# Kernel tuning notes

Hardware: AMD Instinct MI355X
Metric: run time of the kernel (lower is better)

## Reference

```python
import jax, jax.numpy as jnp
import numpy as np
import math

B, S, HID = 1, 2048, 1024
H = 16
D = HID // H          # head_dim = 64
M = 128               # RFF num_features
SIGMA = 1.0
ALPHA = 0.9
NORMALIZE = True


def setup_inputs() -> dict:
    key = jax.random.key(0)
    ks = jax.random.split(key, 12)
    s = 1.0 / math.sqrt(HID)  # nn.Linear default-ish init scale
    inp = {
        "hidden_states": jax.random.normal(ks[0], (B, S, HID), dtype=jnp.float32),
        "attention_mask": jnp.zeros((B, 1, 1, S), dtype=jnp.float32),  # 0 = attend
        "Wq": jax.random.uniform(ks[1], (HID, HID), minval=-s, maxval=s, dtype=jnp.float32),
        "bq": jnp.zeros((HID,), dtype=jnp.float32),
        "Wk": jax.random.uniform(ks[2], (HID, HID), minval=-s, maxval=s, dtype=jnp.float32),
        "bk": jnp.zeros((HID,), dtype=jnp.float32),
        "Wv": jax.random.uniform(ks[3], (HID, HID), minval=-s, maxval=s, dtype=jnp.float32),
        "bv": jnp.zeros((HID,), dtype=jnp.float32),
        "Wo": jax.random.uniform(ks[4], (HID, HID), minval=-s, maxval=s, dtype=jnp.float32),
        "bo": jnp.zeros((HID,), dtype=jnp.float32),
        # RFF kernel params per head: omega ~ N(0, 1/sigma^2), phase b ~ U[0, 2pi]
        "omega": jax.random.normal(ks[5], (H, D, M), dtype=jnp.float32) / SIGMA,
        "rff_b": jax.random.uniform(ks[6], (H, M), minval=0.0, maxval=2.0 * math.pi, dtype=jnp.float32),
    }
    return inp


def _heads(x):
    # (B, S, HID) -> (B, H, S, D)
    return x.reshape(B, S, H, D).transpose(0, 2, 1, 3)


def _phi(x, omega, rff_b):
    # x: (B, H, S, D) -> (B, H, S, M) random Fourier features
    proj = jnp.einsum("bhsd,hdm->bhsm", x, omega) + rff_b[None, :, None, :]
    phi = math.sqrt(2.0 / M) * jnp.cos(proj)
    if NORMALIZE:
        phi = phi / (jnp.linalg.norm(phi, axis=-1, keepdims=True) + 1e-6)
    return phi


def reference(hidden_states, attention_mask, Wq, bq, Wk, bk, Wv, bv, Wo, bo, omega, rff_b):
    q = _heads(hidden_states @ Wq.T + bq)   # (B,H,S,D)
    k = _heads(hidden_states @ Wk.T + bk)
    v = _heads(hidden_states @ Wv.T + bv)

    qn = q / (jnp.linalg.norm(q, axis=-1, keepdims=True) + 1e-6)
    kn = k / (jnp.linalg.norm(k, axis=-1, keepdims=True) + 1e-6)

    dot_scores = jnp.einsum("bhqd,bhkd->bhqk", q, k)             # standard QK^T
    kernel_scores = jnp.einsum("bhqm,bhkm->bhqk",
                               _phi(qn, omega, rff_b),
                               _phi(kn, omega, rff_b))            # phi(Q)phi(K)^T

    scores = (ALPHA * dot_scores + (1.0 - ALPHA) * kernel_scores) / math.sqrt(D)
    scores = scores + attention_mask * -10000.0
    weights = jax.nn.softmax(scores, axis=-1)                     # dropout: eval mode (identity)

    context = jnp.einsum("bhqk,bhkd->bhqd", weights, v)
    context = context.transpose(0, 2, 1, 3).reshape(B, S, HID)
    return context @ Wo.T + bo
```

## Files before the change

kernel.cpp:

```cpp
#include <hip/hip_runtime.h>
#include <math.h>

#define S_LEN 2048
#define HID   1024
#define NH    16
#define HD    64
#define NM    128
#define CAUG  192
#define NCH   32

constexpr float ALPHA = 0.9f;

typedef __attribute__((ext_vector_type(8))) short bf16x8;
typedef __attribute__((ext_vector_type(4))) short bf16x4;
typedef __attribute__((ext_vector_type(4))) float f32x4;
typedef __attribute__((ext_vector_type(4))) int   int4v;

#define MFMA(a,b,c) __builtin_amdgcn_mfma_f32_16x16x32_bf16(a,b,c,0,0,0)

static __device__ inline short f2bf(float f) {
    unsigned u = __float_as_uint(f);
    u += 0x7fffu + ((u >> 16) & 1u);
    return (short)(u >> 16);
}
static __device__ inline float bf2f(short s) {
    return __uint_as_float(((unsigned)(unsigned short)s) << 16);
}

__global__ __launch_bounds__(256)
void conv_kernel(const float* __restrict__ hs,
                 const float* __restrict__ Wq, const float* __restrict__ Wk,
                 const float* __restrict__ Wv, const float* __restrict__ Wo,
                 const float* __restrict__ omega,
                 short* __restrict__ hsb, short* __restrict__ wqb, short* __restrict__ wkb,
                 short* __restrict__ wvb, short* __restrict__ wob, short* __restrict__ omtb)
{
    int i = blockIdx.x * 256 + threadIdx.x;
    if (i >= 1605632) return;
    if (i >= 1572864) {
        int j = (i - 1572864) * 4;
        int h = j >> 13, rem = j & 8191;
        int d = rem >> 7, m = rem & 127;
        float4 v = *(const float4*)(omega + j);
        short* dst = omtb + ((h * 128 + m) << 6) + d;
        dst[0]       = f2bf(v.x);
        dst[64]      = f2bf(v.y);
        dst[128]     = f2bf(v.z);
        dst[192]     = f2bf(v.w);
        return;
    }
    const float* src; short* dst; int off;
    if (i < 524288) { src = hs; dst = hsb; off = i; }
    else {
        int j = i - 524288;
        int r = j >> 18;
        off = j & 262143;
        src = (r == 0) ? Wq : (r == 1) ? Wk : (r == 2) ? Wv : Wo;
        dst = (r == 0) ? wqb : (r == 1) ? wkb : (r == 2) ? wvb : wob;
    }
    float4 v = ((const float4*)src)[off];
    bf16x4 o; o[0] = f2bf(v.x); o[1] = f2bf(v.y); o[2] = f2bf(v.z); o[3] = f2bf(v.w);
    ((bf16x4*)dst)[off] = o;
}

__global__ __launch_bounds__(256)
void gemm_mfma(const short* __restrict__ A,
               const short* __restrict__ W0, const float* __restrict__ b0, void* C0,
               const short* __restrict__ W1, const float* __restrict__ b1, void* C1,
               const short* __restrict__ W2, const float* __restrict__ b2, void* C2,
               int m0_, int m1_, int m2_, int Mrows)
{
    const short* W; const float* bias; void* C; int mode;
    if (blockIdx.z == 0)      { W = W0; bias = b0; C = C0; mode = m0_; }
    else if (blockIdx.z == 1) { W = W1; bias = b1; C = C1; mode = m1_; }
    else                      { W = W2; bias = b2; C = C2; mode = m2_; }

    __shared__ short As[64][40];
    __shared__ short Bs[128][40];

    const int tid = threadIdx.x;
    const int wave = tid >> 6, lane = tid & 63;
    const int l15 = lane & 15, l4 = lane >> 4;
    const int wm = wave >> 1, wn = wave & 1;
    const int m0 = blockIdx.y * 64, n0 = blockIdx.x * 128;

    const int srow = tid >> 2;
    const int scol = (tid & 3) * 16;

    f32x4 acc[2][4];
#pragma unroll
    for (int i = 0; i < 2; ++i)
#pragma unroll
        for (int j = 0; j < 4; ++j) acc[i][j] = (f32x4){0.f,0.f,0.f,0.f};

    int4v apre, bpre0, bpre1;
    apre  = *(const int4v*)((const char*)A + (size_t)(m0 + srow) * 2048 + scol);
    bpre0 = *(const int4v*)((const char*)W + (size_t)(n0 + srow) * 2048 + scol);
    bpre1 = *(const int4v*)((const char*)W + (size_t)(n0 + 64 + srow) * 2048 + scol);

    for (int ks = 0; ks < 32; ++ks) {
        __syncthreads();
        *(int4v*)((char*)&As[0][0] + srow * 80 + scol) = apre;
        *(int4v*)((char*)&Bs[0][0] + srow * 80 + scol) = bpre0;
        *(int4v*)((char*)&Bs[0][0] + (64 + srow) * 80 + scol) = bpre1;
        __syncthreads();
        if (ks + 1 < 32) {
            const int kb = (ks + 1) * 64;
            apre  = *(const int4v*)((const char*)A + (size_t)(m0 + srow) * 2048 + kb + scol);
            bpre0 = *(const int4v*)((const char*)W + (size_t)(n0 + srow) * 2048 + kb + scol);
            bpre1 = *(const int4v*)((const char*)W + (size_t)(n0 + 64 + srow) * 2048 + kb + scol);
        }
        bf16x8 af[2], bf[4];
#pragma unroll
        for (int mi = 0; mi < 2; ++mi)
            af[mi] = *(const bf16x8*)((const char*)&As[0][0] + (wm*32 + mi*16 + l15) * 80 + l4*16);
#pragma unroll
        for (int nj = 0; nj < 4; ++nj)
            bf[nj] = *(const bf16x8*)((const char*)&Bs[0][0] + (wn*64 + nj*16 + l15) * 80 + l4*16);
#pragma unroll
        for (int mi = 0; mi < 2; ++mi)
#pragma unroll
            for (int nj = 0; nj < 4; ++nj)
                acc[mi][nj] = MFMA(af[mi], bf[nj], acc[mi][nj]);
    }

#pragma unroll
    for (int nj = 0; nj < 4; ++nj) {
        const int nglob = n0 + wn*64 + nj*16 + l15;
        const float bn = bias[nglob];
#pragma unroll
        for (int mi = 0; mi < 2; ++mi) {
            const int mbase = m0 + wm*32 + mi*16 + l4*4;
            if (mode == 0) {
#pragma unroll
                for (int r = 0; r < 4; ++r)
                    ((short*)C)[(size_t)(mbase + r) * 1024 + nglob] = f2bf(acc[mi][nj][r] + bn);
            } else if (mode == 1) {
                bf16x4 pk;
#pragma unroll
                for (int r = 0; r < 4; ++r) pk[r] = f2bf(acc[mi][nj][r] + bn);
                *(bf16x4*)((short*)C + (size_t)nglob * Mrows + mbase) = pk;
            } else {
#pragma unroll
                for (int r = 0; r < 4; ++r)
                    ((float*)C)[(size_t)(mbase + r) * 1024 + nglob] = acc[mi][nj][r] + bn;
            }
        }
    }
}

__global__ __launch_bounds__(256)
void phi2_kernel(const short* __restrict__ qbuf, const short* __restrict__ kbuf,
                 const short* __restrict__ omtb, const float* __restrict__ rffb,
                 short* __restrict__ Qa, short* __restrict__ Ka)
{
    __shared__ short om[128][72];
    __shared__ float bsh[128];

    const int src = blockIdx.z, h = blockIdx.y;
    const int s0 = blockIdx.x * 64;
    const short* X = src ? kbuf : qbuf;
    short* Out     = src ? Ka : Qa;
    const float fq   = src ? 1.0f : (ALPHA * 0.125f);
    const float fphi = src ? 1.0f : ((1.0f - ALPHA) * 0.125f);

    const int tid = threadIdx.x, wave = tid >> 6, lane = tid & 63;
    const int l15 = lane & 15, l4 = lane >> 4;

    {
        const char* gsrc = (const char*)(omtb + ((size_t)h << 13));
#pragma unroll
        for (int it = 0; it < 4; ++it) {
            int f = tid * 16 + it * 4096;
            int row = f >> 7, colb = f & 127;
            *(int4v*)((char*)&om[0][0] + row * 144 + colb) = *(const int4v*)(gsrc + f);
        }
        if (tid < 128) bsh[tid] = rffb[h * 128 + tid];
    }
    __syncthreads();

    const int srow = s0 + wave * 16 + l15;

    bf16x8 xf[2];
#pragma unroll
    for (int cs = 0; cs < 2; ++cs)
        xf[cs] = *(const bf16x8*)(X + (size_t)srow * HID + h * HD + cs * 32 + l4 * 8);

    float ss = 0.f;
#pragma unroll
    for (int cs = 0; cs < 2; ++cs)
#pragma unroll
        for (int j = 0; j < 8; ++j) { float v = bf2f(xf[cs][j]); ss = fmaf(v, v, ss); }
    ss += __shfl_xor(ss, 16);
    ss += __shfl_xor(ss, 32);
    const float inv = 1.0f / (sqrtf(ss) + 1e-6f);

    bf16x8 qn[2];
#pragma unroll
    for (int cs = 0; cs < 2; ++cs) {
        bf16x8 o, w;
#pragma unroll
        for (int j = 0; j < 8; ++j) {
            float v = bf2f(xf[cs][j]);
            o[j] = f2bf(v * inv);
            w[j] = f2bf(v * fq);
        }
        qn[cs] = o;
        *(bf16x8*)(Out + ((size_t)h * S_LEN + srow) * CAUG + cs * 32 + l4 * 8) = w;
    }

    f32x4 pacc[8];
#pragma unroll
    for (int t = 0; t < 8; ++t) pacc[t] = (f32x4){0.f,0.f,0.f,0.f};
#pragma unroll
    for (int t = 0; t < 8; ++t)
#pragma unroll
        for (int cs = 0; cs < 2; ++cs) {
            bf16x8 bf = *(const bf16x8*)((const char*)&om[0][0] + (t*16 + l15) * 144 + cs*64 + l4*16);
            pacc[t] = MFMA(qn[cs], bf, pacc[t]);
        }

    float ph[8][4];
    float ps[4] = {0.f, 0.f, 0.f, 0.f};
#pragma unroll
    for (int t = 0; t < 8; ++t) {
        const float bv = bsh[t * 16 + l15];
#pragma unroll
        for (int r = 0; r < 4; ++r) {
            float p = pacc[t][r] + bv;
            float c = 0.125f * __cosf(p);
            ph[t][r] = c;
            ps[r] = fmaf(c, c, ps[r]);
        }
    }
#pragma unroll
    for (int r = 0; r < 4; ++r) {
        ps[r] += __shfl_xor(ps[r], 1);
        ps[r] += __shfl_xor(ps[r], 2);
        ps[r] += __shfl_xor(ps[r], 4);
        ps[r] += __shfl_xor(ps[r], 8);
    }
    float inv2[4];
#pragma unroll
    for (int r = 0; r < 4; ++r) inv2[r] = fphi / (sqrtf(ps[r]) + 1e-6f);

#pragma unroll
    for (int t = 0; t < 8; ++t)
#pragma unroll
        for (int r = 0; r < 4; ++r)
            Out[((size_t)h * S_LEN + s0 + wave * 16 + l4 * 4 + r) * CAUG + 64 + t * 16 + l15]
                = f2bf(ph[t][r] * inv2[r]);
}

__global__ __launch_bounds__(256, 2)
void flash_mfma(const short* __restrict__ Qa, const short* __restrict__ Ka,
                const short* __restrict__ vt, const float* __restrict__ mask,
                short* __restrict__ ctxb)
{
    __shared__ char smem[56320];

    const int tid = threadIdx.x;
    const int wave = tid >> 6, lane = tid & 63;
    const int l15 = lane & 15, l4 = lane >> 4;
    const int g = wave >> 1, sub = wave & 1;
    const int h = blockIdx.y;
    const int q0 = blockIdx.x * 64 + sub * 32;

    char* PlW  = smem + wave * 2560;
    char* Kbuf = smem + 10240 + g * 12800;
    char* Vt0  = smem + 35840 + g * 10240;
    char* Vt1  = Vt0 + 5120;

    bf16x8 qf[2][6];
#pragma unroll
    for (int qj = 0; qj < 2; ++qj)
#pragma unroll
        for (int cs = 0; cs < 6; ++cs)
            qf[qj][cs] = *(const bf16x8*)(Qa + ((size_t)h * 2048 + q0 + qj*16 + l15) * CAUG + cs*32 + l4*8);

    f32x4 oacc[4][2];
#pragma unroll
    for (int di = 0; di < 4; ++di)
#pragma unroll
        for (int qj = 0; qj < 2; ++qj) oacc[di][qj] = (f32x4){0.f,0.f,0.f,0.f};
    float lsum[2] = {0.f, 0.f};

    const int t = tid & 127;
    int kr[6], kcb[6], vr[2], vcb[2];
#pragma unroll
    for (int it = 0; it < 6; ++it) { int f = t*16 + it*2048; kr[it] = f/384; kcb[it] = f%384; }
#pragma unroll
    for (int it = 0; it < 2; ++it) { int f = t*16 + it*2048; vr[it] = f/64; vcb[it] = f%64; }

    const char* Kg = (const char*)(Ka + (size_t)h * 2048 * CAUG);
    const char* Vg = (const char*)(vt + (size_t)h * 64 * 2048);
    const int base = g * NCH;

    int4v kpre[6], vpre[2];
    auto loadPre = [&](int kt) {
        const char* kb = Kg + (size_t)kt * 12288;
#pragma unroll
        for (int it = 0; it < 6; ++it)
            kpre[it] = *(const int4v*)(kb + (size_t)kr[it]*384 + kcb[it]);
#pragma unroll
        for (int it = 0; it < 2; ++it)
            vpre[it] = *(const int4v*)(Vg + (size_t)vr[it]*4096 + kt*64 + vcb[it]);
    };

    f32x4 sacc_p[2][2];
    float4 mkp0, mkp1;

    auto softmax_pv = [&](char* Vbuf) {
#pragma unroll
        for (int fi = 0; fi < 2; ++fi) {
            const float4 mk = fi ? mkp1 : mkp0;
            float mv[4] = {mk.x * -10000.f, mk.y * -10000.f, mk.z * -10000.f, mk.w * -10000.f};
#pragma unroll
            for (int qj = 0; qj < 2; ++qj) {
                bf16x4 pk;
#pragma unroll
                for (int r = 0; r < 4; ++r) {
                    float p = __expf(sacc_p[fi][qj][r] + mv[r]);
                    lsum[qj] += p;
                    pk[r] = f2bf(p);
                }
                *(bf16x4*)(PlW + (qj*16 + l15)*80 + fi*32 + l4*8) = pk;
            }
        }
        bf16x8 va[4], pb[2];
#pragma unroll
        for (int di = 0; di < 4; ++di)
            va[di] = *(const bf16x8*)(Vbuf + (di*16 + l15)*80 + l4*16);
#pragma unroll
        for (int qj = 0; qj < 2; ++qj)
            pb[qj] = *(const bf16x8*)(PlW + (qj*16 + l15)*80 + l4*16);
#pragma unroll
        for (int di = 0; di < 4; ++di)
#pragma unroll
            for (int qj = 0; qj < 2; ++qj)
                oacc[di][qj] = MFMA(va[di], pb[qj], oacc[di][qj]);
    };

    loadPre(base);

    for (int i = 0; i < NCH; ++i) {
        const int kt = base + i;
        char* Vcur = (i & 1) ? Vt1 : Vt0;
        __syncthreads();
#pragma unroll
        for (int it = 0; it < 6; ++it)
            *(int4v*)(Kbuf + kr[it]*400 + kcb[it]) = kpre[it];
#pragma unroll
        for (int it = 0; it < 2; ++it)
            *(int4v*)(Vcur + vr[it]*80 + vcb[it]) = vpre[it];
        __syncthreads();

        f32x4 sc[2][2];
#pragma unroll
        for (int fi = 0; fi < 2; ++fi)
#pragma unroll
            for (int qj = 0; qj < 2; ++qj) sc[fi][qj] = (f32x4){0.f,0.f,0.f,0.f};
#pragma unroll
        for (int cs = 0; cs < 6; ++cs) {
            bf16x8 ka[2];
#pragma unroll
            for (int fi = 0; fi < 2; ++fi)
                ka[fi] = *(const bf16x8*)(Kbuf + (fi*16 + l15)*400 + cs*64 + l4*16);
#pragma unroll
            for (int fi = 0; fi < 2; ++fi)
#pragma unroll
                for (int qj = 0; qj < 2; ++qj)
                    sc[fi][qj] = MFMA(ka[fi], qf[qj][cs], sc[fi][qj]);
        }
        float4 mkc0 = *(const float4*)&mask[kt*32 + l4*4];
        float4 mkc1 = *(const float4*)&mask[kt*32 + 16 + l4*4];

        if (i + 1 < NCH) loadPre(kt + 1);

        if (i > 0) softmax_pv((i & 1) ? Vt0 : Vt1);

#pragma unroll
        for (int fi = 0; fi < 2; ++fi)
#pragma unroll
            for (int qj = 0; qj < 2; ++qj) sacc_p[fi][qj] = sc[fi][qj];
        mkp0 = mkc0; mkp1 = mkc1;
    }
    softmax_pv(Vt1);

#pragma unroll
    for (int qj = 0; qj < 2; ++qj) {
        lsum[qj] += __shfl_xor(lsum[qj], 16);
        lsum[qj] += __shfl_xor(lsum[qj], 32);
    }

    __syncthreads();
    float* scrO = (float*)(smem + 10240);
    float* scrL = (float*)(smem + 27648);
    if (g == 1) {
#pragma unroll
        for (int qj = 0; qj < 2; ++qj) {
#pragma unroll
            for (int di = 0; di < 4; ++di)
                *(f32x4*)&scrO[(size_t)(sub*32 + qj*16 + l15)*68 + di*16 + l4*4] = oacc[di][qj];
            if (l4 == 0) scrL[sub*32 + qj*16 + l15] = lsum[qj];
        }
    }
    __syncthreads();
    if (g == 0) {
#pragma unroll
        for (int qj = 0; qj < 2; ++qj) {
            const float l = lsum[qj] + scrL[sub*32 + qj*16 + l15];
            const float inv = 1.0f / l;
            const int s = q0 + qj*16 + l15;
#pragma unroll
            for (int di = 0; di < 4; ++di) {
                f32x4 o2 = *(const f32x4*)&scrO[(size_t)(sub*32 + qj*16 + l15)*68 + di*16 + l4*4];
                bf16x4 ob;
#pragma unroll
                for (int r = 0; r < 4; ++r) ob[r] = f2bf((oacc[di][qj][r] + o2[r]) * inv);
                *(bf16x4*)(ctxb + (size_t)s * HID + h*64 + di*16 + l4*4) = ob;
            }
        }
    }
}

extern "C" void kernel_launch(void* const* d_in, const int* in_sizes, int n_in,
                              void* d_out, int out_size, void* d_ws, size_t ws_size,
                              hipStream_t stream)
{
    const float* hs    = (const float*)d_in[0];
    const float* mask  = (const float*)d_in[1];
    const float* Wq    = (const float*)d_in[2];
    const float* bq    = (const float*)d_in[3];
    const float* Wk    = (const float*)d_in[4];
    const float* bk    = (const float*)d_in[5];
    const float* Wv    = (const float*)d_in[6];
    const float* bv    = (const float*)d_in[7];
    const float* Wo    = (const float*)d_in[8];
    const float* bo    = (const float*)d_in[9];
    const float* omega = (const float*)d_in[10];
    const float* rffb  = (const float*)d_in[11];
    float* out = (float*)d_out;

    short* wsS = (short*)d_ws;
    short* hsb = wsS;
    short* wqb = hsb + 2097152;
    short* wkb = wqb + 1048576;
    short* wvb = wkb + 1048576;
    short* wob = wvb + 1048576;
    short* qb  = wob + 1048576;
    short* kb  = qb  + 2097152;
    short* vtb = kb  + 2097152;
    short* ctxb= vtb + 2097152;
    short* QaB = ctxb+ 2097152;
    short* KaB = QaB + 6291456;
    short* omtb= KaB + 6291456;

    conv_kernel<<<6272, 256, 0, stream>>>(hs, Wq, Wk, Wv, Wo, omega,
                                          hsb, wqb, wkb, wvb, wob, omtb);
    gemm_mfma<<<dim3(8, 32, 3), 256, 0, stream>>>(hsb, wqb, bq, qb, wkb, bk, kb, wvb, bv, vtb,
                                                  0, 0, 1, S_LEN);
    phi2_kernel<<<dim3(32, 16, 2), 256, 0, stream>>>(qb, kb, omtb, rffb, QaB, KaB);
    flash_mfma<<<dim3(32, 16), 256, 0, stream>>>(QaB, KaB, vtb, mask, ctxb);
    gemm_mfma<<<dim3(8, 32, 1), 256, 0, stream>>>(ctxb, wob, bo, out, wob, bo, out, wob, bo, out,
                                                  2, 2, 2, S_LEN);
}
```

Before: 119.1 us.

## Split flash attention keys across four waves with per-wave private K tiles

Restructures the attention kernel so each of the four waves handles all 64 queries of the block over its own quarter of the key range, in place of two wave groups that each covered half the queries and half the keys. Each wave now stages its K tile in its own XOR-swizzled LDS region, which removes the per-chunk __syncthreads. V fragments are loaded straight from global memory into registers, and the next K tile is written into LDS half by half while the current one is consumed. This cuts block-wide barriers and LDS bank conflicts, at the cost of more registers (64 query rows per wave) and a four-way reduction of partial outputs at the end.

```diff
diff --git a/kernel.cpp b/kernel.cpp
--- a/kernel.cpp
+++ b/kernel.cpp
@@ -7,7 +7,6 @@
 #define HD    64
 #define NM    128
 #define CAUG  192
-#define NCH   32
 
 constexpr float ALPHA = 0.9f;
 
@@ -257,168 +256,158 @@
                 const short* __restrict__ vt, const float* __restrict__ mask,
                 short* __restrict__ ctxb)
 {
-    __shared__ char smem[56320];
+    __shared__ char smem[65536];
 
     const int tid = threadIdx.x;
     const int wave = tid >> 6, lane = tid & 63;
     const int l15 = lane & 15, l4 = lane >> 4;
-    const int g = wave >> 1, sub = wave & 1;
     const int h = blockIdx.y;
-    const int q0 = blockIdx.x * 64 + sub * 32;
-
-    char* PlW  = smem + wave * 2560;
-    char* Kbuf = smem + 10240 + g * 12800;
-    char* Vt0  = smem + 35840 + g * 10240;
-    char* Vt1  = Vt0 + 5120;
-
-    bf16x8 qf[2][6];
-#pragma unroll
-    for (int qj = 0; qj < 2; ++qj)
+    const int q0 = blockIdx.x * 64;
+
+    char* Kbuf = smem + wave * 12288;
+    char* Pb   = smem + 49152 + wave * 4096;
+
+    bf16x8 qf[4][6];
+#pragma unroll
+    for (int qj = 0; qj < 4; ++qj)
 #pragma unroll
         for (int cs = 0; cs < 6; ++cs)
             qf[qj][cs] = *(const bf16x8*)(Qa + ((size_t)h * 2048 + q0 + qj*16 + l15) * CAUG + cs*32 + l4*8);
 
-    f32x4 oacc[4][2];
+    f32x4 oacc[4][4];
 #pragma unroll
     for (int di = 0; di < 4; ++di)
 #pragma unroll
-        for (int qj = 0; qj < 2; ++qj) oacc[di][qj] = (f32x4){0.f,0.f,0.f,0.f};
-    float lsum[2] = {0.f, 0.f};
-
-    const int t = tid & 127;
-    int kr[6], kcb[6], vr[2], vcb[2];
-#pragma unroll
-    for (int it = 0; it < 6; ++it) { int f = t*16 + it*2048; kr[it] = f/384; kcb[it] = f%384; }
-#pragma unroll
-    for (int it = 0; it < 2; ++it) { int f = t*16 + it*2048; vr[it] = f/64; vcb[it] = f%64; }
+        for (int qj = 0; qj < 4; ++qj) oacc[di][qj] = (f32x4){0.f,0.f,0.f,0.f};
+    float lsum[4] = {0.f, 0.f, 0.f, 0.f};
 
     const char* Kg = (const char*)(Ka + (size_t)h * 2048 * CAUG);
     const char* Vg = (const char*)(vt + (size_t)h * 64 * 2048);
-    const int base = g * NCH;
-
-    int4v kpre[6], vpre[2];
-    auto loadPre = [&](int kt) {
-        const char* kb = Kg + (size_t)kt * 12288;
+    const int c0 = wave * 16;
+
+    int wrA[6];
+#pragma unroll
+    for (int it = 0; it < 6; ++it) {
+        int p = it * 1024 + lane * 16;
+        int row = p / 384;
+        int col = p - row * 384;
+        wrA[it] = row * 384 + (col ^ ((row & 7) << 4));
+    }
+
+    int4v kpre[6];
+    bf16x8 va[4];
+
+    auto loadKhalf = [&](int kt, int half) {
+        const char* kb = Kg + (size_t)kt * 12288 + half * 6144;
 #pragma unroll
         for (int it = 0; it < 6; ++it)
-            kpre[it] = *(const int4v*)(kb + (size_t)kr[it]*384 + kcb[it]);
-#pragma unroll
-        for (int it = 0; it < 2; ++it)
-            vpre[it] = *(const int4v*)(Vg + (size_t)vr[it]*4096 + kt*64 + vcb[it]);
+            kpre[it] = *(const int4v*)(kb + it * 1024 + lane * 16);
     };
-
-    f32x4 sacc_p[2][2];
-    float4 mkp0, mkp1;
-
-    auto softmax_pv = [&](char* Vbuf) {
+    auto writeKhalf = [&](int half) {
+        char* b = Kbuf + half * 6144;
+#pragma unroll
+        for (int it = 0; it < 6; ++it)
+            *(int4v*)(b + wrA[it]) = kpre[it];
+    };
+    auto loadV = [&](int kt) {
+#pragma unroll
+        for (int di = 0; di < 4; ++di)
+            va[di] = *(const bf16x8*)(Vg + (size_t)(di*16 + l15)*4096 + kt*64 + l4*16);
+    };
+
+    loadKhalf(c0, 0); writeKhalf(0);
+    loadKhalf(c0, 1); writeKhalf(1);
+    loadV(c0);
+
+    for (int i = 0; i < 16; ++i) {
+        const int kt = c0 + i;
+        const bool more = (i + 1 < 16);
+        if (more) loadKhalf(kt + 1, 0);
+
 #pragma unroll
         for (int fi = 0; fi < 2; ++fi) {
-            const float4 mk = fi ? mkp1 : mkp0;
+            f32x4 sacc[4];
+#pragma unroll
+            for (int qj = 0; qj < 4; ++qj) sacc[qj] = (f32x4){0.f,0.f,0.f,0.f};
+            const int r = fi * 16 + l15;
+            const int sw = (l15 & 7) << 4;
+#pragma unroll
+            for (int cs = 0; cs < 6; ++cs) {
+                bf16x8 ka = *(const bf16x8*)(Kbuf + r * 384 + ((cs*64 + l4*16) ^ sw));
+#pragma unroll
+                for (int qj = 0; qj < 4; ++qj)
+                    sacc[qj] = MFMA(ka, qf[qj][cs], sacc[qj]);
+            }
+            float4 mk = *(const float4*)&mask[kt*32 + fi*16 + l4*4];
             float mv[4] = {mk.x * -10000.f, mk.y * -10000.f, mk.z * -10000.f, mk.w * -10000.f};
 #pragma unroll
-            for (int qj = 0; qj < 2; ++qj) {
+            for (int qj = 0; qj < 4; ++qj) {
                 bf16x4 pk;
 #pragma unroll
-                for (int r = 0; r < 4; ++r) {
-                    float p = __expf(sacc_p[fi][qj][r] + mv[r]);
+                for (int rr = 0; rr < 4; ++rr) {
+                    float p = __expf(sacc[qj][rr] + mv[rr]);
                     lsum[qj] += p;
-                    pk[r] = f2bf(p);
+                    pk[rr] = f2bf(p);
                 }
-                *(bf16x4*)(PlW + (qj*16 + l15)*80 + fi*32 + l4*8) = pk;
+                const int prow = qj*16 + l15;
+                *(bf16x4*)(Pb + prow*64 + ((fi*32 + l4*8) ^ ((prow & 3) << 4))) = pk;
             }
-        }
-        bf16x8 va[4], pb[2];
-#pragma unroll
-        for (int di = 0; di < 4; ++di)
-            va[di] = *(const bf16x8*)(Vbuf + (di*16 + l15)*80 + l4*16);
-#pragma unroll
-        for (int qj = 0; qj < 2; ++qj)
-            pb[qj] = *(const bf16x8*)(PlW + (qj*16 + l15)*80 + l4*16);
-#pragma unroll
-        for (int di = 0; di < 4; ++di)
-#pragma unroll
-            for (int qj = 0; qj < 2; ++qj)
-                oacc[di][qj] = MFMA(va[di], pb[qj], oacc[di][qj]);
-    };
-
-    loadPre(base);
-
-    for (int i = 0; i < NCH; ++i) {
-        const int kt = base + i;
-        char* Vcur = (i & 1) ? Vt1 : Vt0;
-        __syncthreads();
-#pragma unroll
-        for (int it = 0; it < 6; ++it)
-            *(int4v*)(Kbuf + kr[it]*400 + kcb[it]) = kpre[it];
-#pragma unroll
-        for (int it = 0; it < 2; ++it)
-            *(int4v*)(Vcur + vr[it]*80 + vcb[it]) = vpre[it];
-        __syncthreads();
-
-        f32x4 sc[2][2];
-#pragma unroll
-        for (int fi = 0; fi < 2; ++fi)
-#pragma unroll
-            for (int qj = 0; qj < 2; ++qj) sc[fi][qj] = (f32x4){0.f,0.f,0.f,0.f};
-#pragma unroll
-        for (int cs = 0; cs < 6; ++cs) {
-            bf16x8 ka[2];
-#pragma unroll
-            for (int fi = 0; fi < 2; ++fi)
-                ka[fi] = *(const bf16x8*)(Kbuf + (fi*16 + l15)*400 + cs*64 + l4*16);
-#pragma unroll
-            for (int fi = 0; fi < 2; ++fi)
-#pragma unroll
-                for (int qj = 0; qj < 2; ++qj)
-                    sc[fi][qj] = MFMA(ka[fi], qf[qj][cs], sc[fi][qj]);
-        }
-        float4 mkc0 = *(const float4*)&mask[kt*32 + l4*4];
-        float4 mkc1 = *(const float4*)&mask[kt*32 + 16 + l4*4];
-
-        if (i + 1 < NCH) loadPre(kt + 1);
-
-        if (i > 0) softmax_pv((i & 1) ? Vt0 : Vt1);
-
-#pragma unroll
-        for (int fi = 0; fi < 2; ++fi)
-#pragma unroll
-            for (int qj = 0; qj < 2; ++qj) sacc_p[fi][qj] = sc[fi][qj];
-        mkp0 = mkc0; mkp1 = mkc1;
-    }
-    softmax_pv(Vt1);
-
-#pragma unroll
-    for (int qj = 0; qj < 2; ++qj) {
+            asm volatile("" ::: "memory");
+            if (more) {
+                writeKhalf(fi);
+                if (fi == 0) loadKhalf(kt + 1, 1);
+            }
+        }
+
+#pragma unroll
+        for (int qj = 0; qj < 4; ++qj) {
+            const int prow = qj*16 + l15;
+            bf16x8 pb = *(const bf16x8*)(Pb + prow*64 + ((l4*16) ^ ((prow & 3) << 4)));
+#pragma unroll
+            for (int di = 0; di < 4; ++di)
+                oacc[di][qj] = MFMA(va[di], pb, oacc[di][qj]);
+        }
+        if (more) loadV(kt + 1);
+    }
+
+#pragma unroll
+    for (int qj = 0; qj < 4; ++qj) {
         lsum[qj] += __shfl_xor(lsum[qj], 16);
         lsum[qj] += __shfl_xor(lsum[qj], 32);
     }
 
     __syncthreads();
-    float* scrO = (float*)(smem + 10240);
-    float* scrL = (float*)(smem + 27648);
-    if (g == 1) {
-#pragma unroll
-        for (int qj = 0; qj < 2; ++qj) {
+    float* scrO = (float*)smem;
+    float* scrL = (float*)(smem + 49152);
+    if (wave > 0) {
+#pragma unroll
+        for (int qj = 0; qj < 4; ++qj) {
+            const int q = qj*16 + l15;
 #pragma unroll
             for (int di = 0; di < 4; ++di)
-                *(f32x4*)&scrO[(size_t)(sub*32 + qj*16 + l15)*68 + di*16 + l4*4] = oacc[di][qj];
-            if (l4 == 0) scrL[sub*32 + qj*16 + l15] = lsum[qj];
+                *(f32x4*)&scrO[(size_t)((wave-1)*64 + q)*64 + di*16 + l4*4] = oacc[di][qj];
+            if (l4 == 0) scrL[(wave-1)*64 + q] = lsum[qj];
         }
     }
     __syncthreads();
-    if (g == 0) {
-#pragma unroll
-        for (int qj = 0; qj < 2; ++qj) {
-            const float l = lsum[qj] + scrL[sub*32 + qj*16 + l15];
+    if (wave == 0) {
+#pragma unroll
+        for (int qj = 0; qj < 4; ++qj) {
+            const int q = qj*16 + l15;
+            float l = lsum[qj];
+#pragma unroll
+            for (int k = 0; k < 3; ++k) l += scrL[k*64 + q];
             const float inv = 1.0f / l;
-            const int s = q0 + qj*16 + l15;
 #pragma unroll
             for (int di = 0; di < 4; ++di) {
-                f32x4 o2 = *(const f32x4*)&scrO[(size_t)(sub*32 + qj*16 + l15)*68 + di*16 + l4*4];
+                f32x4 o = oacc[di][qj];
+#pragma unroll
+                for (int k = 0; k < 3; ++k)
+                    o += *(const f32x4*)&scrO[(size_t)(k*64 + q)*64 + di*16 + l4*4];
                 bf16x4 ob;
 #pragma unroll
-                for (int r = 0; r < 4; ++r) ob[r] = f2bf((oacc[di][qj][r] + o2[r]) * inv);
-                *(bf16x4*)(ctxb + (size_t)s * HID + h*64 + di*16 + l4*4) = ob;
+                for (int r = 0; r < 4; ++r) ob[r] = f2bf(o[r] * inv);
+                *(bf16x4*)(ctxb + (size_t)(q0 + q) * HID + h*64 + di*16 + l4*4) = ob;
             }
         }
     }
```

After: 131.5 us. 1.1x slower.

## Split attention keys across grid blocks with separate merge kernel

Applied to the files above, without the earlier changes.

Replaces the in-block two-group key split with a four-way split across the grid: each 128-thread block handles 16 key tiles, writes unnormalized bf16 partial outputs and row sums to workspace, and a new merge kernel sums and normalizes them. LDS layout switches from padded rows to XOR-swizzled rows, and the register prefetch/software pipeline of softmax and PV is removed. This raises block count and occupancy and cuts shared memory per block, at the cost of an extra kernel launch, extra global traffic for partials, and bf16 rounding of partial sums.

```diff
diff --git a/kernel.cpp b/kernel.cpp
--- a/kernel.cpp
+++ b/kernel.cpp
@@ -7,7 +7,7 @@
 #define HD    64
 #define NM    128
 #define CAUG  192
-#define NCH   32
+#define KSPL  4
 
 constexpr float ALPHA = 0.9f;
 
@@ -252,24 +252,22 @@
                 = f2bf(ph[t][r] * inv2[r]);
 }
 
-__global__ __launch_bounds__(256, 2)
+__global__ __launch_bounds__(128, 4)
 void flash_mfma(const short* __restrict__ Qa, const short* __restrict__ Ka,
                 const short* __restrict__ vt, const float* __restrict__ mask,
-                short* __restrict__ ctxb)
-{
-    __shared__ char smem[56320];
+                short* __restrict__ Opart, float* __restrict__ Lpart)
+{
+    __shared__ char smem[20480];
 
     const int tid = threadIdx.x;
     const int wave = tid >> 6, lane = tid & 63;
     const int l15 = lane & 15, l4 = lane >> 4;
-    const int g = wave >> 1, sub = wave & 1;
-    const int h = blockIdx.y;
-    const int q0 = blockIdx.x * 64 + sub * 32;
-
-    char* PlW  = smem + wave * 2560;
-    char* Kbuf = smem + 10240 + g * 12800;
-    char* Vt0  = smem + 35840 + g * 10240;
-    char* Vt1  = Vt0 + 5120;
+    const int h = blockIdx.y, ksp = blockIdx.z;
+    const int q0 = blockIdx.x * 64 + wave * 32;
+
+    char* Kbuf = smem;
+    char* Vbuf = smem + 12288;
+    char* Pb   = smem + 16384 + wave * 2048;
 
     bf16x8 qf[2][6];
 #pragma unroll
@@ -285,107 +283,94 @@
         for (int qj = 0; qj < 2; ++qj) oacc[di][qj] = (f32x4){0.f,0.f,0.f,0.f};
     float lsum[2] = {0.f, 0.f};
 
-    const int t = tid & 127;
-    int kr[6], kcb[6], vr[2], vcb[2];
-#pragma unroll
-    for (int it = 0; it < 6; ++it) { int f = t*16 + it*2048; kr[it] = f/384; kcb[it] = f%384; }
-#pragma unroll
-    for (int it = 0; it < 2; ++it) { int f = t*16 + it*2048; vr[it] = f/64; vcb[it] = f%64; }
+    int gK[6], wrK[6];
+#pragma unroll
+    for (int it = 0; it < 6; ++it) {
+        int f = tid * 16 + it * 2048;
+        int row = f / 384, col = f - row * 384;
+        gK[it] = f;
+        wrK[it] = row * 384 + (col ^ ((row & 7) << 4));
+    }
+    int gVrow[2], gVcol[2], wrV[2];
+#pragma unroll
+    for (int it = 0; it < 2; ++it) {
+        int f = tid * 16 + it * 2048;
+        int row = f >> 6, col = f & 63;
+        gVrow[it] = row; gVcol[it] = col;
+        wrV[it] = row * 64 + (col ^ ((row & 3) << 4));
+    }
 
     const char* Kg = (const char*)(Ka + (size_t)h * 2048 * CAUG);
     const char* Vg = (const char*)(vt + (size_t)h * 64 * 2048);
-    const int base = g * NCH;
-
-    int4v kpre[6], vpre[2];
-    auto loadPre = [&](int kt) {
+    const int base = ksp * 16;
+    const int swP = (l15 & 3) << 4;
+    const int swK = (l15 & 7) << 4;
+
+    for (int i = 0; i < 16; ++i) {
+        const int kt = base + i;
+        int4v kv[6], vv[2];
         const char* kb = Kg + (size_t)kt * 12288;
 #pragma unroll
         for (int it = 0; it < 6; ++it)
-            kpre[it] = *(const int4v*)(kb + (size_t)kr[it]*384 + kcb[it]);
+            kv[it] = *(const int4v*)(kb + gK[it]);
 #pragma unroll
         for (int it = 0; it < 2; ++it)
-            vpre[it] = *(const int4v*)(Vg + (size_t)vr[it]*4096 + kt*64 + vcb[it]);
-    };
-
-    f32x4 sacc_p[2][2];
-    float4 mkp0, mkp1;
-
-    auto softmax_pv = [&](char* Vbuf) {
+            vv[it] = *(const int4v*)(Vg + (size_t)gVrow[it] * 4096 + kt * 64 + gVcol[it]);
+        __syncthreads();
+#pragma unroll
+        for (int it = 0; it < 6; ++it) *(int4v*)(Kbuf + wrK[it]) = kv[it];
+#pragma unroll
+        for (int it = 0; it < 2; ++it) *(int4v*)(Vbuf + wrV[it]) = vv[it];
+        __syncthreads();
+
+        f32x4 sacc[2][2];
+#pragma unroll
+        for (int fi = 0; fi < 2; ++fi)
+#pragma unroll
+            for (int qj = 0; qj < 2; ++qj) sacc[fi][qj] = (f32x4){0.f,0.f,0.f,0.f};
+#pragma unroll
+        for (int cs = 0; cs < 6; ++cs) {
+            bf16x8 ka[2];
+#pragma unroll
+            for (int fi = 0; fi < 2; ++fi)
+                ka[fi] = *(const bf16x8*)(Kbuf + (fi*16 + l15)*384 + ((cs*64 + l4*16) ^ swK));
+#pragma unroll
+            for (int fi = 0; fi < 2; ++fi)
+#pragma unroll
+                for (int qj = 0; qj < 2; ++qj)
+                    sacc[fi][qj] = MFMA(ka[fi], qf[qj][cs], sacc[fi][qj]);
+        }
 #pragma unroll
         for (int fi = 0; fi < 2; ++fi) {
-            const float4 mk = fi ? mkp1 : mkp0;
+            float4 mk = *(const float4*)&mask[kt*32 + fi*16 + l4*4];
             float mv[4] = {mk.x * -10000.f, mk.y * -10000.f, mk.z * -10000.f, mk.w * -10000.f};
 #pragma unroll
             for (int qj = 0; qj < 2; ++qj) {
                 bf16x4 pk;
 #pragma unroll
                 for (int r = 0; r < 4; ++r) {
-                    float p = __expf(sacc_p[fi][qj][r] + mv[r]);
+                    float p = __expf(sacc[fi][qj][r] + mv[r]);
                     lsum[qj] += p;
                     pk[r] = f2bf(p);
                 }
-                *(bf16x4*)(PlW + (qj*16 + l15)*80 + fi*32 + l4*8) = pk;
+                *(bf16x4*)(Pb + (qj*16 + l15)*64 + ((fi*32 + l4*8) ^ swP)) = pk;
             }
         }
-        bf16x8 va[4], pb[2];
-#pragma unroll
-        for (int di = 0; di < 4; ++di)
-            va[di] = *(const bf16x8*)(Vbuf + (di*16 + l15)*80 + l4*16);
-#pragma unroll
-        for (int qj = 0; qj < 2; ++qj)
-            pb[qj] = *(const bf16x8*)(PlW + (qj*16 + l15)*80 + l4*16);
-#pragma unroll
-        for (int di = 0; di < 4; ++di)
+        {
+            bf16x8 pb[2];
 #pragma unroll
             for (int qj = 0; qj < 2; ++qj)
-                oacc[di][qj] = MFMA(va[di], pb[qj], oacc[di][qj]);
-    };
-
-    loadPre(base);
-
-    for (int i = 0; i < NCH; ++i) {
-        const int kt = base + i;
-        char* Vcur = (i & 1) ? Vt1 : Vt0;
-        __syncthreads();
-#pragma unroll
-        for (int it = 0; it < 6; ++it)
-            *(int4v*)(Kbuf + kr[it]*400 + kcb[it]) = kpre[it];
-#pragma unroll
-        for (int it = 0; it < 2; ++it)
-            *(int4v*)(Vcur + vr[it]*80 + vcb[it]) = vpre[it];
-        __syncthreads();
-
-        f32x4 sc[2][2];
-#pragma unroll
-        for (int fi = 0; fi < 2; ++fi)
-#pragma unroll
-            for (int qj = 0; qj < 2; ++qj) sc[fi][qj] = (f32x4){0.f,0.f,0.f,0.f};
-#pragma unroll
-        for (int cs = 0; cs < 6; ++cs) {
-            bf16x8 ka[2];
-#pragma unroll
-            for (int fi = 0; fi < 2; ++fi)
-                ka[fi] = *(const bf16x8*)(Kbuf + (fi*16 + l15)*400 + cs*64 + l4*16);
-#pragma unroll
-            for (int fi = 0; fi < 2; ++fi)
+                pb[qj] = *(const bf16x8*)(Pb + (qj*16 + l15)*64 + ((l4*16) ^ swP));
+#pragma unroll
+            for (int di = 0; di < 4; ++di) {
+                const int vrow = di*16 + l15;
+                bf16x8 va = *(const bf16x8*)(Vbuf + vrow*64 + ((l4*16) ^ ((vrow & 3) << 4)));
 #pragma unroll
                 for (int qj = 0; qj < 2; ++qj)
-                    sc[fi][qj] = MFMA(ka[fi], qf[qj][cs], sc[fi][qj]);
-        }
-        float4 mkc0 = *(const float4*)&mask[kt*32 + l4*4];
-        float4 mkc1 = *(const float4*)&mask[kt*32 + 16 + l4*4];
-
-        if (i + 1 < NCH) loadPre(kt + 1);
-
-        if (i > 0) softmax_pv((i & 1) ? Vt0 : Vt1);
-
-#pragma unroll
-        for (int fi = 0; fi < 2; ++fi)
-#pragma unroll
-            for (int qj = 0; qj < 2; ++qj) sacc_p[fi][qj] = sc[fi][qj];
-        mkp0 = mkc0; mkp1 = mkc1;
-    }
-    softmax_pv(Vt1);
+                    oacc[di][qj] = MFMA(va, pb[qj], oacc[di][qj]);
+            }
+        }
+    }
 
 #pragma unroll
     for (int qj = 0; qj < 2; ++qj) {
@@ -393,35 +378,45 @@
         lsum[qj] += __shfl_xor(lsum[qj], 32);
     }
 
-    __syncthreads();
-    float* scrO = (float*)(smem + 10240);
-    float* scrL = (float*)(smem + 27648);
-    if (g == 1) {
-#pragma unroll
-        for (int qj = 0; qj < 2; ++qj) {
-#pragma unroll
-            for (int di = 0; di < 4; ++di)
-                *(f32x4*)&scrO[(size_t)(sub*32 + qj*16 + l15)*68 + di*16 + l4*4] = oacc[di][qj];
-            if (l4 == 0) scrL[sub*32 + qj*16 + l15] = lsum[qj];
-        }
-    }
-    __syncthreads();
-    if (g == 0) {
-#pragma unroll
-        for (int qj = 0; qj < 2; ++qj) {
-            const float l = lsum[qj] + scrL[sub*32 + qj*16 + l15];
-            const float inv = 1.0f / l;
-            const int s = q0 + qj*16 + l15;
-#pragma unroll
-            for (int di = 0; di < 4; ++di) {
-                f32x4 o2 = *(const f32x4*)&scrO[(size_t)(sub*32 + qj*16 + l15)*68 + di*16 + l4*4];
-                bf16x4 ob;
-#pragma unroll
-                for (int r = 0; r < 4; ++r) ob[r] = f2bf((oacc[di][qj][r] + o2[r]) * inv);
-                *(bf16x4*)(ctxb + (size_t)s * HID + h*64 + di*16 + l4*4) = ob;
-            }
-        }
-    }
+    const size_t obase = (size_t)(ksp * NH + h) * 2048 + q0;
+#pragma unroll
+    for (int qj = 0; qj < 2; ++qj) {
+        const size_t orow = obase + qj*16 + l15;
+#pragma unroll
+        for (int di = 0; di < 4; ++di) {
+            bf16x4 ob;
+#pragma unroll
+            for (int r = 0; r < 4; ++r) ob[r] = f2bf(oacc[di][qj][r]);
+            *(bf16x4*)(Opart + orow * 64 + di*16 + l4*4) = ob;
+        }
+        if (l4 == 0) Lpart[orow] = lsum[qj];
+    }
+}
+
+__global__ __launch_bounds__(256)
+void merge_kernel(const short* __restrict__ Opart, const float* __restrict__ Lpart,
+                  short* __restrict__ ctxb)
+{
+    int tt = blockIdx.x * 256 + threadIdx.x;
+    int e = tt * 4;
+    int d = e & 63;
+    int q = (e >> 6) & 2047;
+    int h = e >> 17;
+    float acc[4] = {0.f, 0.f, 0.f, 0.f};
+    float L = 0.f;
+#pragma unroll
+    for (int s = 0; s < KSPL; ++s) {
+        size_t idx = (size_t)(s * NH + h) * 2048 + q;
+        bf16x4 a = *(const bf16x4*)(Opart + idx * 64 + d);
+        L += Lpart[idx];
+#pragma unroll
+        for (int r = 0; r < 4; ++r) acc[r] += bf2f(a[r]);
+    }
+    float inv = 1.0f / L;
+    bf16x4 o;
+#pragma unroll
+    for (int r = 0; r < 4; ++r) o[r] = f2bf(acc[r] * inv);
+    *(bf16x4*)(ctxb + (size_t)q * 1024 + h * 64 + d) = o;
 }
 
 extern "C" void kernel_launch(void* const* d_in, const int* in_sizes, int n_in,
@@ -442,26 +437,29 @@
     const float* rffb  = (const float*)d_in[11];
     float* out = (float*)d_out;
 
-    short* wsS = (short*)d_ws;
-    short* hsb = wsS;
-    short* wqb = hsb + 2097152;
-    short* wkb = wqb + 1048576;
-    short* wvb = wkb + 1048576;
-    short* wob = wvb + 1048576;
-    short* qb  = wob + 1048576;
-    short* kb  = qb  + 2097152;
-    short* vtb = kb  + 2097152;
-    short* ctxb= vtb + 2097152;
-    short* QaB = ctxb+ 2097152;
-    short* KaB = QaB + 6291456;
-    short* omtb= KaB + 6291456;
+    short* wsS  = (short*)d_ws;
+    short* hsb  = wsS;
+    short* wqb  = hsb + 2097152;
+    short* wkb  = wqb + 1048576;
+    short* wvb  = wkb + 1048576;
+    short* wob  = wvb + 1048576;
+    short* qb   = wob + 1048576;
+    short* kb   = qb  + 2097152;
+    short* vtb  = kb  + 2097152;
+    short* ctxb = vtb + 2097152;
+    short* QaB  = ctxb+ 2097152;
+    short* KaB  = QaB + 6291456;
+    short* omtb = KaB + 6291456;
+    short* OpS  = omtb+ 131072;
+    float* LpF  = (float*)(OpS + 8388608);
 
     conv_kernel<<<6272, 256, 0, stream>>>(hs, Wq, Wk, Wv, Wo, omega,
                                           hsb, wqb, wkb, wvb, wob, omtb);
     gemm_mfma<<<dim3(8, 32, 3), 256, 0, stream>>>(hsb, wqb, bq, qb, wkb, bk, kb, wvb, bv, vtb,
                                                   0, 0, 1, S_LEN);
     phi2_kernel<<<dim3(32, 16, 2), 256, 0, stream>>>(qb, kb, omtb, rffb, QaB, KaB);
-    flash_mfma<<<dim3(32, 16), 256, 0, stream>>>(QaB, KaB, vtb, mask, ctxb);
+    flash_mfma<<<dim3(32, 16, KSPL), 128, 0, stream>>>(QaB, KaB, vtb, mask, OpS, LpF);
+    merge_kernel<<<2048, 256, 0, stream>>>(OpS, LpF, ctxb);
     gemm_mfma<<<dim3(8, 32, 1), 256, 0, stream>>>(ctxb, wob, bo, out, wob, bo, out, wob, bo, out,
                                                   2, 2, 2, S_LEN);
 }
```

New measurement: 135.8 us. 14.0% more time.
